# Performance work log

Hardware: AMD Instinct MI355X
Metric: run time of the kernel (lower is better)

The kernel has to match this reference:

```python
import jax, jax.numpy as jnp
import numpy as np

S = 64.0
M = 0.5
EPS = 1e-07
NORM_EPS = 1e-12  # matches torch F.normalize default eps
B, D, C = 512, 512, 64000


def _l2_normalize(a, axis=-1):
    n = jnp.sqrt(jnp.sum(a * a, axis=axis, keepdims=True))
    return a / jnp.maximum(n, NORM_EPS)


def setup_inputs() -> dict:
    key = jax.random.key(0)
    kx, ky, kw = jax.random.split(key, 3)
    x = jax.random.normal(kx, (B, D), dtype=jnp.float32)
    y = jax.random.randint(ky, (B,), 0, C, dtype=jnp.int64)
    # kaiming_uniform-ish init: bound = sqrt(6 / fan_in)
    bound = np.sqrt(6.0 / D).astype(np.float32)
    W = jax.random.uniform(kw, (C, D), dtype=jnp.float32, minval=-bound, maxval=bound)
    return {"x": x, "y": y, "W": W}


def reference(x, y, W):
    # cosine similarities: [B, C]
    theta = _l2_normalize(x) @ _l2_normalize(W).T
    # target logit per row
    tgt = jnp.take_along_axis(theta, y[:, None], axis=1)[:, 0]  # [B]
    numerator = S * jnp.cos(jnp.arccos(jnp.clip(tgt, -1.0 + EPS, 1.0 - EPS)) + M)
    # sum of exp(s*theta) over non-target classes (mask out target column)
    is_tgt = jnp.arange(C, dtype=y.dtype)[None, :] == y[:, None]  # [B, C]
    excl_sum = jnp.sum(jnp.where(is_tgt, 0.0, jnp.exp(S * theta)), axis=1)  # [B]
    denominator = jnp.exp(numerator) + excl_sum
    return -jnp.mean(numerator - jnp.log(denominator))
```

## Files before the change

### kernel.cpp

```cpp
#include <hip/hip_runtime.h>


#define B_N 512
#define D_N 512
#define C_N 64000
#define S_SCALE 64.0f
#define MARGIN 0.5f
#define EPS_C 1e-7f
#define NREP 16

typedef unsigned short ushort_t;
typedef __attribute__((ext_vector_type(8))) short short8;
typedef __attribute__((ext_vector_type(4))) float floatx4;
typedef __attribute__((ext_vector_type(4))) float fvec4;

__device__ __forceinline__ ushort_t f2bf(float f) {
    unsigned int u = __float_as_uint(f);
    u += 0x7fffu + ((u >> 16) & 1u);
    return (ushort_t)(u >> 16);
}

__global__ void xprep_kernel(const float* __restrict__ x,
                             ushort_t* __restrict__ xnT,
                             float* __restrict__ rowsumR) {
    int b = blockIdx.x;
    int t = threadIdx.x;
    if (b == 128) {
#pragma unroll
        for (int i = 0; i < NREP * B_N / 256; ++i)
            rowsumR[i * 256 + t] = 0.0f;
        return;
    }
    int row  = b * 4 + (t >> 6);
    int lane = t & 63;
    const float4* p = (const float4*)(x + (size_t)row * D_N);
    float4 v0 = p[lane * 2];
    float4 v1 = p[lane * 2 + 1];
    float ss = v0.x*v0.x + v0.y*v0.y + v0.z*v0.z + v0.w*v0.w
             + v1.x*v1.x + v1.y*v1.y + v1.z*v1.z + v1.w*v1.w;
#pragma unroll
    for (int off = 32; off > 0; off >>= 1) ss += __shfl_xor(ss, off);
    float sc = 1.0f / fmaxf(sqrtf(ss), 1e-12f);
    uint4 o;
    o.x = (unsigned)f2bf(v0.x*sc) | ((unsigned)f2bf(v0.y*sc) << 16);
    o.y = (unsigned)f2bf(v0.z*sc) | ((unsigned)f2bf(v0.w*sc) << 16);
    o.z = (unsigned)f2bf(v1.x*sc) | ((unsigned)f2bf(v1.y*sc) << 16);
    o.w = (unsigned)f2bf(v1.z*sc) | ((unsigned)f2bf(v1.w*sc) << 16);
    *((uint4*)(xnT + ((size_t)(lane << 9) + row) * 8)) = o;
}

__global__ __launch_bounds__(512, 4)
void gemm_fused_kernel(const float* __restrict__ W,
                       const ushort_t* __restrict__ xnT,
                       const int* __restrict__ y,
                       float* __restrict__ rowsumR,
                       float* __restrict__ tgt) {
    __shared__ ushort_t sW[64 * 512];

    int t    = threadIdx.x;
    int lane = t & 63;
    int w    = t >> 6;
    int lq   = lane >> 4;
    int lc   = lane & 15;
    int cn0  = blockIdx.x * 64;

#pragma unroll
    for (int rr = 0; rr < 8; ++rr) {
        int row = w * 8 + rr;
        const fvec4* p = (const fvec4*)(W + (size_t)(cn0 + row) * D_N);
        fvec4 a = __builtin_nontemporal_load(p + lane * 2);
        fvec4 b = __builtin_nontemporal_load(p + lane * 2 + 1);
        float ss = a.x*a.x + a.y*a.y + a.z*a.z + a.w*a.w
                 + b.x*b.x + b.y*b.y + b.z*b.z + b.w*b.w;
#pragma unroll
        for (int off = 32; off > 0; off >>= 1) ss += __shfl_xor(ss, off);
        float sc = 1.0f / fmaxf(sqrtf(ss), 1e-12f);
        uint4 o;
        o.x = (unsigned)f2bf(a.x*sc) | ((unsigned)f2bf(a.y*sc) << 16);
        o.y = (unsigned)f2bf(a.z*sc) | ((unsigned)f2bf(a.w*sc) << 16);
        o.z = (unsigned)f2bf(b.x*sc) | ((unsigned)f2bf(b.y*sc) << 16);
        o.w = (unsigned)f2bf(b.z*sc) | ((unsigned)f2bf(b.w*sc) << 16);
        int kc = lane;
        int rs = row ^ (kc & 7);
        *((uint4*)(sW + kc * 512 + rs * 8)) = o;
    }
    __syncthreads();

    floatx4 acc[4][4];
#pragma unroll
    for (int i = 0; i < 4; i++)
#pragma unroll
        for (int j = 0; j < 4; j++) acc[i][j] = (floatx4){0.f, 0.f, 0.f, 0.f};

    const ushort_t* apT[4];
#pragma unroll
    for (int tm = 0; tm < 4; tm++)
        apT[tm] = xnT + ((size_t)lq * 512 + w * 64 + tm * 16 + lc) * 8;

    short8 af[4];
#pragma unroll
    for (int tm = 0; tm < 4; tm++) af[tm] = *(const short8*)(apT[tm]);

    for (int k = 0; k < 16; ++k) {
        short8 afn[4];
        if (k < 15) {
#pragma unroll
            for (int tm = 0; tm < 4; tm++)
                afn[tm] = *(const short8*)(apT[tm] + (k + 1) * 16384);
        }
        int kc = k * 4 + lq;
        short8 bfr[4];
#pragma unroll
        for (int tn = 0; tn < 4; tn++) {
            int rs = (tn * 16 + lc) ^ (kc & 7);
            bfr[tn] = *(const short8*)(sW + kc * 512 + rs * 8);
        }
#pragma unroll
        for (int tm = 0; tm < 4; tm++)
#pragma unroll
            for (int tn = 0; tn < 4; tn++)
                acc[tm][tn] = __builtin_amdgcn_mfma_f32_16x16x32_bf16(
                    af[tm], bfr[tn], acc[tm][tn], 0, 0, 0);
        if (k < 15) {
#pragma unroll
            for (int tm = 0; tm < 4; tm++) af[tm] = afn[tm];
        }
    }

    __syncthreads();
    float* rowacc = (float*)sW;
#pragma unroll
    for (int tm = 0; tm < 4; tm++) {
#pragma unroll
        for (int r = 0; r < 4; r++) {
            int lrow = w * 64 + tm * 16 + lq * 4 + r;
            int yv   = y[lrow];
            float esum = 0.0f;
#pragma unroll
            for (int tn = 0; tn < 4; tn++) {
                int gcol = cn0 + tn * 16 + lc;
                float theta = acc[tm][tn][r];
                if (gcol == yv) {
                    tgt[lrow] = theta;
                } else {
                    esum += __expf(S_SCALE * theta);
                }
            }
#pragma unroll
            for (int off = 1; off < 16; off <<= 1) esum += __shfl_xor(esum, off);
            if (lc == 0) rowacc[lrow] = esum;
        }
    }
    __syncthreads();
    atomicAdd(&rowsumR[(blockIdx.x & (NREP - 1)) * B_N + t], rowacc[t]);
}

__global__ void finalize_kernel(const float* __restrict__ rowsumR,
                                const float* __restrict__ tgt,
                                float* __restrict__ out) {
    __shared__ float red[256];
    int t = threadIdx.x;
    float s = 0.0f;
    for (int r = t; r < B_N; r += 256) {
        float rs = 0.0f;
#pragma unroll
        for (int i = 0; i < NREP; ++i) rs += rowsumR[i * B_N + r];
        float tv = tgt[r];
        tv = fminf(fmaxf(tv, -1.0f + EPS_C), 1.0f - EPS_C);
        float num = S_SCALE * cosf(acosf(tv) + MARGIN);
        float den = expf(num) + rs;
        s += num - logf(den);
    }
    red[t] = s;
    __syncthreads();
    for (int o = 128; o > 0; o >>= 1) {
        if (t < o) red[t] += red[t + o];
        __syncthreads();
    }
    if (t == 0) out[0] = -red[0] / (float)B_N;
}

extern "C" void kernel_launch(void* const* d_in, const int* in_sizes, int n_in,
                              void* d_out, int out_size, void* d_ws, size_t ws_size,
                              hipStream_t stream) {
    const float* x = (const float*)d_in[0];
    const int*   y = (const int*)d_in[1];
    const float* W = (const float*)d_in[2];
    float* out = (float*)d_out;

    char* ws = (char*)d_ws;
    ushort_t* xnT   = (ushort_t*)ws;
    float* rowsumR  = (float*)(ws + 524288);
    float* tgt      = rowsumR + NREP * B_N;

    xprep_kernel<<<129, 256, 0, stream>>>(x, xnT, rowsumR);
    gemm_fused_kernel<<<C_N / 64, 512, 0, stream>>>(W, xnT, y, rowsumR, tgt);
    finalize_kernel<<<1, 256, 0, stream>>>(rowsumR, tgt, out);
}
```

Before: 221.5 us.

## Process four class tiles per block with double-buffered W prefetch

```diff
diff --git a/kernel.cpp b/kernel.cpp
--- a/kernel.cpp
+++ b/kernel.cpp
@@ -8,6 +8,8 @@
 #define MARGIN 0.5f
 #define EPS_C 1e-7f
 #define NREP 16
+#define TPB 4
+#define GRID_GEMM 250
 
 typedef unsigned short ushort_t;
 typedef __attribute__((ext_vector_type(8))) short short8;
@@ -49,25 +51,36 @@
     *((uint4*)(xnT + ((size_t)(lane << 9) + row) * 8)) = o;
 }
 
-__global__ __launch_bounds__(512, 4)
+__global__ __launch_bounds__(512, 2)
 void gemm_fused_kernel(const float* __restrict__ W,
                        const ushort_t* __restrict__ xnT,
                        const int* __restrict__ y,
                        float* __restrict__ rowsumR,
                        float* __restrict__ tgt) {
-    __shared__ ushort_t sW[64 * 512];
-
-    int t    = threadIdx.x;
-    int lane = t & 63;
-    int w    = t >> 6;
-    int lq   = lane >> 4;
-    int lc   = lane & 15;
-    int cn0  = blockIdx.x * 64;
+    __shared__ ushort_t sW[2][64 * 512];
+
+    int t     = threadIdx.x;
+    int lane  = t & 63;
+    int w     = t >> 6;
+    int lq    = lane >> 4;
+    int lc    = lane & 15;
+    int cbase = blockIdx.x * (TPB * 64);
+
+    const ushort_t* apT[4];
+#pragma unroll
+    for (int tm = 0; tm < 4; tm++)
+        apT[tm] = xnT + ((size_t)lq * 512 + w * 64 + tm * 16 + lc) * 8;
+
+    float esum[4][4];
+#pragma unroll
+    for (int tm = 0; tm < 4; tm++)
+#pragma unroll
+        for (int r = 0; r < 4; r++) esum[tm][r] = 0.0f;
 
 #pragma unroll
     for (int rr = 0; rr < 8; ++rr) {
         int row = w * 8 + rr;
-        const fvec4* p = (const fvec4*)(W + (size_t)(cn0 + row) * D_N);
+        const fvec4* p = (const fvec4*)(W + (size_t)(cbase + row) * D_N);
         fvec4 a = __builtin_nontemporal_load(p + lane * 2);
         fvec4 b = __builtin_nontemporal_load(p + lane * 2 + 1);
         float ss = a.x*a.x + a.y*a.y + a.z*a.z + a.w*a.w
@@ -82,77 +95,126 @@
         o.w = (unsigned)f2bf(b.z*sc) | ((unsigned)f2bf(b.w*sc) << 16);
         int kc = lane;
         int rs = row ^ (kc & 7);
-        *((uint4*)(sW + kc * 512 + rs * 8)) = o;
+        *((uint4*)(&sW[0][kc * 512 + rs * 8])) = o;
     }
     __syncthreads();
 
-    floatx4 acc[4][4];
-#pragma unroll
-    for (int i = 0; i < 4; i++)
-#pragma unroll
-        for (int j = 0; j < 4; j++) acc[i][j] = (floatx4){0.f, 0.f, 0.f, 0.f};
-
-    const ushort_t* apT[4];
-#pragma unroll
-    for (int tm = 0; tm < 4; tm++)
-        apT[tm] = xnT + ((size_t)lq * 512 + w * 64 + tm * 16 + lc) * 8;
-
-    short8 af[4];
-#pragma unroll
-    for (int tm = 0; tm < 4; tm++) af[tm] = *(const short8*)(apT[tm]);
-
-    for (int k = 0; k < 16; ++k) {
-        short8 afn[4];
-        if (k < 15) {
+    int cur = 0;
+    for (int tt = 0; tt < TPB; ++tt) {
+        const int  cn0     = cbase + tt * 64;
+        const bool notlast = (tt < TPB - 1);
+        const ushort_t* sWc = sW[cur];
+        ushort_t*       sWn = sW[cur ^ 1];
+        const int  nb      = cn0 + 64;
+
+        floatx4 acc[4][4];
+#pragma unroll
+        for (int i = 0; i < 4; i++)
+#pragma unroll
+            for (int j = 0; j < 4; j++) acc[i][j] = (floatx4){0.f, 0.f, 0.f, 0.f};
+
+        short8 af[4];
+#pragma unroll
+        for (int tm = 0; tm < 4; tm++) af[tm] = *(const short8*)(apT[tm]);
+
+        fvec4 wA[8], wB[8];
+
+#pragma unroll
+        for (int k = 0; k < 16; ++k) {
+            short8 afn[4];
+            if (k < 15) {
+#pragma unroll
+                for (int tm = 0; tm < 4; tm++)
+                    afn[tm] = *(const short8*)(apT[tm] + (k + 1) * 16384);
+            }
+            if (notlast && (k == 1 || k == 3 || k == 5 || k == 7)) {
+                const int bi = (k - 1) >> 1;
+#pragma unroll
+                for (int rx = 0; rx < 2; ++rx) {
+                    int row = w * 8 + bi * 2 + rx;
+                    const fvec4* p = (const fvec4*)(W + (size_t)(nb + row) * D_N);
+                    wA[bi * 2 + rx] = __builtin_nontemporal_load(p + lane * 2);
+                    wB[bi * 2 + rx] = __builtin_nontemporal_load(p + lane * 2 + 1);
+                }
+            }
+            const int kc = k * 4 + lq;
+            short8 bfr[4];
+#pragma unroll
+            for (int tn = 0; tn < 4; tn++) {
+                int rs = (tn * 16 + lc) ^ (kc & 7);
+                bfr[tn] = *(const short8*)(&sWc[kc * 512 + rs * 8]);
+            }
 #pragma unroll
             for (int tm = 0; tm < 4; tm++)
-                afn[tm] = *(const short8*)(apT[tm] + (k + 1) * 16384);
+#pragma unroll
+                for (int tn = 0; tn < 4; tn++)
+                    acc[tm][tn] = __builtin_amdgcn_mfma_f32_16x16x32_bf16(
+                        af[tm], bfr[tn], acc[tm][tn], 0, 0, 0);
+            if (notlast && (k == 9 || k == 11 || k == 13 || k == 15)) {
+                const int bi = (k - 9) >> 1;
+#pragma unroll
+                for (int rx = 0; rx < 2; ++rx) {
+                    int row = w * 8 + bi * 2 + rx;
+                    fvec4 a = wA[bi * 2 + rx];
+                    fvec4 b = wB[bi * 2 + rx];
+                    float ss = a.x*a.x + a.y*a.y + a.z*a.z + a.w*a.w
+                             + b.x*b.x + b.y*b.y + b.z*b.z + b.w*b.w;
+#pragma unroll
+                    for (int off = 32; off > 0; off >>= 1) ss += __shfl_xor(ss, off);
+                    float sc = 1.0f / fmaxf(sqrtf(ss), 1e-12f);
+                    uint4 o;
+                    o.x = (unsigned)f2bf(a.x*sc) | ((unsigned)f2bf(a.y*sc) << 16);
+                    o.y = (unsigned)f2bf(a.z*sc) | ((unsigned)f2bf(a.w*sc) << 16);
+                    o.z = (unsigned)f2bf(b.x*sc) | ((unsigned)f2bf(b.y*sc) << 16);
+                    o.w = (unsigned)f2bf(b.z*sc) | ((unsigned)f2bf(b.w*sc) << 16);
+                    int kcs = lane;
+                    int rs  = row ^ (kcs & 7);
+                    *((uint4*)(&sWn[kcs * 512 + rs * 8])) = o;
+                }
+            }
+            if (k < 15) {
+#pragma unroll
+                for (int tm = 0; tm < 4; tm++) af[tm] = afn[tm];
+            }
         }
-        int kc = k * 4 + lq;
-        short8 bfr[4];
-#pragma unroll
-        for (int tn = 0; tn < 4; tn++) {
-            int rs = (tn * 16 + lc) ^ (kc & 7);
-            bfr[tn] = *(const short8*)(sW + kc * 512 + rs * 8);
+
+#pragma unroll
+        for (int tm = 0; tm < 4; tm++) {
+#pragma unroll
+            for (int r = 0; r < 4; r++) {
+                int grow = w * 64 + tm * 16 + lq * 4 + r;
+                int yv   = y[grow];
+                float es = 0.0f;
+#pragma unroll
+                for (int tn = 0; tn < 4; tn++) {
+                    int gcol = cn0 + tn * 16 + lc;
+                    float theta = acc[tm][tn][r];
+                    if (gcol == yv) {
+                        tgt[grow] = theta;
+                    } else {
+                        es += __expf(S_SCALE * theta);
+                    }
+                }
+                esum[tm][r] += es;
+            }
         }
-#pragma unroll
-        for (int tm = 0; tm < 4; tm++)
-#pragma unroll
-            for (int tn = 0; tn < 4; tn++)
-                acc[tm][tn] = __builtin_amdgcn_mfma_f32_16x16x32_bf16(
-                    af[tm], bfr[tn], acc[tm][tn], 0, 0, 0);
-        if (k < 15) {
-#pragma unroll
-            for (int tm = 0; tm < 4; tm++) af[tm] = afn[tm];
+        __syncthreads();
+        cur ^= 1;
+    }
+
+#pragma unroll
+    for (int tm = 0; tm < 4; tm++) {
+#pragma unroll
+        for (int r = 0; r < 4; r++) {
+            float e = esum[tm][r];
+#pragma unroll
+            for (int off = 1; off < 16; off <<= 1) e += __shfl_xor(e, off);
+            if (lc == 0) {
+                int grow = w * 64 + tm * 16 + lq * 4 + r;
+                atomicAdd(&rowsumR[(blockIdx.x & (NREP - 1)) * B_N + grow], e);
+            }
         }
     }
-
-    __syncthreads();
-    float* rowacc = (float*)sW;
-#pragma unroll
-    for (int tm = 0; tm < 4; tm++) {
-#pragma unroll
-        for (int r = 0; r < 4; r++) {
-            int lrow = w * 64 + tm * 16 + lq * 4 + r;
-            int yv   = y[lrow];
-            float esum = 0.0f;
-#pragma unroll
-            for (int tn = 0; tn < 4; tn++) {
-                int gcol = cn0 + tn * 16 + lc;
-                float theta = acc[tm][tn][r];
-                if (gcol == yv) {
-                    tgt[lrow] = theta;
-                } else {
-                    esum += __expf(S_SCALE * theta);
-                }
-            }
-#pragma unroll
-            for (int off = 1; off < 16; off <<= 1) esum += __shfl_xor(esum, off);
-            if (lc == 0) rowacc[lrow] = esum;
-        }
-    }
-    __syncthreads();
-    atomicAdd(&rowsumR[(blockIdx.x & (NREP - 1)) * B_N + t], rowacc[t]);
 }
 
 __global__ void finalize_kernel(const float* __restrict__ rowsumR,
@@ -194,6 +256,6 @@
     float* tgt      = rowsumR + NREP * B_N;
 
     xprep_kernel<<<129, 256, 0, stream>>>(x, xnT, rowsumR);
-    gemm_fused_kernel<<<C_N / 64, 512, 0, stream>>>(W, xnT, y, rowsumR, tgt);
+    gemm_fused_kernel<<<GRID_GEMM, 512, 0, stream>>>(W, xnT, y, rowsumR, tgt);
     finalize_kernel<<<1, 256, 0, stream>>>(rowsumR, tgt, out);
 }
```

Result: slower. 396.6 us (+79.1%).

## Shrink GEMM tile to 32 classes per block and defer W normalization

Applied to the files above, without the earlier changes.

```diff
diff --git a/kernel.cpp b/kernel.cpp
--- a/kernel.cpp
+++ b/kernel.cpp
@@ -8,6 +8,8 @@
 #define MARGIN 0.5f
 #define EPS_C 1e-7f
 #define NREP 16
+#define TILE_C 32
+#define GRID_GEMM 2000
 
 typedef unsigned short ushort_t;
 typedef __attribute__((ext_vector_type(8))) short short8;
@@ -49,20 +51,22 @@
     *((uint4*)(xnT + ((size_t)(lane << 9) + row) * 8)) = o;
 }
 
-__global__ __launch_bounds__(512, 4)
+__global__ __launch_bounds__(256, 4)
 void gemm_fused_kernel(const float* __restrict__ W,
                        const ushort_t* __restrict__ xnT,
                        const int* __restrict__ y,
                        float* __restrict__ rowsumR,
                        float* __restrict__ tgt) {
-    __shared__ ushort_t sW[64 * 512];
+    __shared__ ushort_t sW[64 * 256];
+    __shared__ float    norms2[TILE_C];
 
     int t    = threadIdx.x;
     int lane = t & 63;
     int w    = t >> 6;
     int lq   = lane >> 4;
     int lc   = lane & 15;
-    int cn0  = blockIdx.x * 64;
+    int cn0  = blockIdx.x * TILE_C;
+    int rep  = blockIdx.x & (NREP - 1);
 
 #pragma unroll
     for (int rr = 0; rr < 8; ++rr) {
@@ -74,85 +78,82 @@
                  + b.x*b.x + b.y*b.y + b.z*b.z + b.w*b.w;
 #pragma unroll
         for (int off = 32; off > 0; off >>= 1) ss += __shfl_xor(ss, off);
-        float sc = 1.0f / fmaxf(sqrtf(ss), 1e-12f);
         uint4 o;
-        o.x = (unsigned)f2bf(a.x*sc) | ((unsigned)f2bf(a.y*sc) << 16);
-        o.y = (unsigned)f2bf(a.z*sc) | ((unsigned)f2bf(a.w*sc) << 16);
-        o.z = (unsigned)f2bf(b.x*sc) | ((unsigned)f2bf(b.y*sc) << 16);
-        o.w = (unsigned)f2bf(b.z*sc) | ((unsigned)f2bf(b.w*sc) << 16);
-        int kc = lane;
-        int rs = row ^ (kc & 7);
-        *((uint4*)(sW + kc * 512 + rs * 8)) = o;
+        o.x = (unsigned)f2bf(a.x) | ((unsigned)f2bf(a.y) << 16);
+        o.y = (unsigned)f2bf(a.z) | ((unsigned)f2bf(a.w) << 16);
+        o.z = (unsigned)f2bf(b.x) | ((unsigned)f2bf(b.y) << 16);
+        o.w = (unsigned)f2bf(b.z) | ((unsigned)f2bf(b.w) << 16);
+        *((uint4*)(&sW[lane * 256 + (row ^ (lane & 7)) * 8])) = o;
+        if (lane == 0) norms2[row] = ss;
     }
     __syncthreads();
 
-    floatx4 acc[4][4];
-#pragma unroll
-    for (int i = 0; i < 4; i++)
-#pragma unroll
-        for (int j = 0; j < 4; j++) acc[i][j] = (floatx4){0.f, 0.f, 0.f, 0.f};
-
-    const ushort_t* apT[4];
-#pragma unroll
-    for (int tm = 0; tm < 4; tm++)
-        apT[tm] = xnT + ((size_t)lq * 512 + w * 64 + tm * 16 + lc) * 8;
-
-    short8 af[4];
-#pragma unroll
-    for (int tm = 0; tm < 4; tm++) af[tm] = *(const short8*)(apT[tm]);
+    const ushort_t* abase = xnT + ((size_t)lq * 512 + (size_t)w * 128 + lc) * 8;
+
+    floatx4 acc[8][2];
+#pragma unroll
+    for (int i = 0; i < 8; i++)
+#pragma unroll
+        for (int j = 0; j < 2; j++) acc[i][j] = (floatx4){0.f, 0.f, 0.f, 0.f};
+
+    short8 af[8], afn[8];
+#pragma unroll
+    for (int tm = 0; tm < 8; tm++)
+        af[tm] = *(const short8*)(abase + tm * 128);
 
     for (int k = 0; k < 16; ++k) {
-        short8 afn[4];
         if (k < 15) {
 #pragma unroll
-            for (int tm = 0; tm < 4; tm++)
-                afn[tm] = *(const short8*)(apT[tm] + (k + 1) * 16384);
+            for (int tm = 0; tm < 8; tm++)
+                afn[tm] = *(const short8*)(abase + (size_t)(k + 1) * 16384 + tm * 128);
         }
         int kc = k * 4 + lq;
-        short8 bfr[4];
-#pragma unroll
-        for (int tn = 0; tn < 4; tn++) {
+        short8 bfr[2];
+#pragma unroll
+        for (int tn = 0; tn < 2; tn++) {
             int rs = (tn * 16 + lc) ^ (kc & 7);
-            bfr[tn] = *(const short8*)(sW + kc * 512 + rs * 8);
-        }
-#pragma unroll
-        for (int tm = 0; tm < 4; tm++)
-#pragma unroll
-            for (int tn = 0; tn < 4; tn++)
+            bfr[tn] = *(const short8*)(&sW[kc * 256 + rs * 8]);
+        }
+#pragma unroll
+        for (int tm = 0; tm < 8; tm++)
+#pragma unroll
+            for (int tn = 0; tn < 2; tn++)
                 acc[tm][tn] = __builtin_amdgcn_mfma_f32_16x16x32_bf16(
                     af[tm], bfr[tn], acc[tm][tn], 0, 0, 0);
         if (k < 15) {
 #pragma unroll
-            for (int tm = 0; tm < 4; tm++) af[tm] = afn[tm];
-        }
-    }
-
-    __syncthreads();
-    float* rowacc = (float*)sW;
-#pragma unroll
-    for (int tm = 0; tm < 4; tm++) {
+            for (int tm = 0; tm < 8; tm++) af[tm] = afn[tm];
+        }
+    }
+
+    float rn[2];
+#pragma unroll
+    for (int tn = 0; tn < 2; tn++)
+        rn[tn] = 1.0f / fmaxf(sqrtf(norms2[tn * 16 + lc]), 1e-12f);
+
+#pragma unroll
+    for (int tm = 0; tm < 8; tm++) {
 #pragma unroll
         for (int r = 0; r < 4; r++) {
-            int lrow = w * 64 + tm * 16 + lq * 4 + r;
-            int yv   = y[lrow];
-            float esum = 0.0f;
-#pragma unroll
-            for (int tn = 0; tn < 4; tn++) {
+            int grow = w * 128 + tm * 16 + lq * 4 + r;
+            int yv   = y[grow];
+            float es = 0.0f;
+#pragma unroll
+            for (int tn = 0; tn < 2; tn++) {
                 int gcol = cn0 + tn * 16 + lc;
-                float theta = acc[tm][tn][r];
+                float theta = acc[tm][tn][r] * rn[tn];
                 if (gcol == yv) {
-                    tgt[lrow] = theta;
+                    tgt[grow] = theta;
                 } else {
-                    esum += __expf(S_SCALE * theta);
+                    es += __expf(S_SCALE * theta);
                 }
             }
 #pragma unroll
-            for (int off = 1; off < 16; off <<= 1) esum += __shfl_xor(esum, off);
-            if (lc == 0) rowacc[lrow] = esum;
-        }
-    }
-    __syncthreads();
-    atomicAdd(&rowsumR[(blockIdx.x & (NREP - 1)) * B_N + t], rowacc[t]);
+            for (int off = 1; off < 16; off <<= 1) es += __shfl_xor(es, off);
+            if (lc == 0)
+                atomicAdd(&rowsumR[rep * B_N + grow], es);
+        }
+    }
 }
 
 __global__ void finalize_kernel(const float* __restrict__ rowsumR,
@@ -194,6 +195,6 @@
     float* tgt      = rowsumR + NREP * B_N;
 
     xprep_kernel<<<129, 256, 0, stream>>>(x, xnT, rowsumR);
-    gemm_fused_kernel<<<C_N / 64, 512, 0, stream>>>(W, xnT, y, rowsumR, tgt);
+    gemm_fused_kernel<<<GRID_GEMM, 256, 0, stream>>>(W, xnT, y, rowsumR, tgt);
     finalize_kernel<<<1, 256, 0, stream>>>(rowsumR, tgt, out);
 }
```

After: 263.9 us. +19.2%, slower.

## Use persistent warp-specialized GEMM blocks with double-buffered W tiles

Applied to the files above, without the earlier changes.

```diff
diff --git a/kernel.cpp b/kernel.cpp
--- a/kernel.cpp
+++ b/kernel.cpp
@@ -8,6 +8,10 @@
 #define MARGIN 0.5f
 #define EPS_C 1e-7f
 #define NREP 16
+#define TPB 4
+#define GRID_GEMM 250
+#define NCONS 8
+#define NTHREADS 640
 
 typedef unsigned short ushort_t;
 typedef __attribute__((ext_vector_type(8))) short short8;
@@ -49,110 +53,160 @@
     *((uint4*)(xnT + ((size_t)(lane << 9) + row) * 8)) = o;
 }
 
-__global__ __launch_bounds__(512, 4)
+__global__ __launch_bounds__(NTHREADS, 2)
 void gemm_fused_kernel(const float* __restrict__ W,
                        const ushort_t* __restrict__ xnT,
                        const int* __restrict__ y,
                        float* __restrict__ rowsumR,
                        float* __restrict__ tgt) {
-    __shared__ ushort_t sW[64 * 512];
-
-    int t    = threadIdx.x;
-    int lane = t & 63;
-    int w    = t >> 6;
-    int lq   = lane >> 4;
-    int lc   = lane & 15;
-    int cn0  = blockIdx.x * 64;
-
-#pragma unroll
-    for (int rr = 0; rr < 8; ++rr) {
-        int row = w * 8 + rr;
-        const fvec4* p = (const fvec4*)(W + (size_t)(cn0 + row) * D_N);
-        fvec4 a = __builtin_nontemporal_load(p + lane * 2);
-        fvec4 b = __builtin_nontemporal_load(p + lane * 2 + 1);
-        float ss = a.x*a.x + a.y*a.y + a.z*a.z + a.w*a.w
-                 + b.x*b.x + b.y*b.y + b.z*b.z + b.w*b.w;
-#pragma unroll
-        for (int off = 32; off > 0; off >>= 1) ss += __shfl_xor(ss, off);
-        float sc = 1.0f / fmaxf(sqrtf(ss), 1e-12f);
-        uint4 o;
-        o.x = (unsigned)f2bf(a.x*sc) | ((unsigned)f2bf(a.y*sc) << 16);
-        o.y = (unsigned)f2bf(a.z*sc) | ((unsigned)f2bf(a.w*sc) << 16);
-        o.z = (unsigned)f2bf(b.x*sc) | ((unsigned)f2bf(b.y*sc) << 16);
-        o.w = (unsigned)f2bf(b.z*sc) | ((unsigned)f2bf(b.w*sc) << 16);
-        int kc = lane;
-        int rs = row ^ (kc & 7);
-        *((uint4*)(sW + kc * 512 + rs * 8)) = o;
+    __shared__ ushort_t sW[2][64 * 512];
+    __shared__ float    norms2[2][64];
+
+    const int t    = threadIdx.x;
+    const int lane = t & 63;
+    const int w    = t >> 6;
+    const int lq   = lane >> 4;
+    const int lc   = lane & 15;
+    const int cbase = blockIdx.x * (TPB * 64);
+    const int rep   = blockIdx.x & (NREP - 1);
+
+    if (w < NCONS) {
+#pragma unroll 4
+        for (int rr = 0; rr < 8; ++rr) {
+            int row = w * 8 + rr;
+            const fvec4* p = (const fvec4*)(W + (size_t)(cbase + row) * D_N);
+            fvec4 a = __builtin_nontemporal_load(p + lane * 2);
+            fvec4 b = __builtin_nontemporal_load(p + lane * 2 + 1);
+            float ss = a.x*a.x + a.y*a.y + a.z*a.z + a.w*a.w
+                     + b.x*b.x + b.y*b.y + b.z*b.z + b.w*b.w;
+#pragma unroll
+            for (int off = 32; off > 0; off >>= 1) ss += __shfl_xor(ss, off);
+            uint4 o;
+            o.x = (unsigned)f2bf(a.x) | ((unsigned)f2bf(a.y) << 16);
+            o.y = (unsigned)f2bf(a.z) | ((unsigned)f2bf(a.w) << 16);
+            o.z = (unsigned)f2bf(b.x) | ((unsigned)f2bf(b.y) << 16);
+            o.w = (unsigned)f2bf(b.z) | ((unsigned)f2bf(b.w) << 16);
+            *((uint4*)(&sW[0][lane * 512 + (row ^ (lane & 7)) * 8])) = o;
+            if (lane == 0) norms2[0][row] = ss;
+        }
     }
     __syncthreads();
 
-    floatx4 acc[4][4];
-#pragma unroll
-    for (int i = 0; i < 4; i++)
-#pragma unroll
-        for (int j = 0; j < 4; j++) acc[i][j] = (floatx4){0.f, 0.f, 0.f, 0.f};
-
-    const ushort_t* apT[4];
-#pragma unroll
-    for (int tm = 0; tm < 4; tm++)
-        apT[tm] = xnT + ((size_t)lq * 512 + w * 64 + tm * 16 + lc) * 8;
-
-    short8 af[4];
-#pragma unroll
-    for (int tm = 0; tm < 4; tm++) af[tm] = *(const short8*)(apT[tm]);
-
-    for (int k = 0; k < 16; ++k) {
-        short8 afn[4];
-        if (k < 15) {
+    int cur = 0;
+#pragma unroll 1
+    for (int tt = 0; tt < TPB; ++tt) {
+        const int cn0 = cbase + tt * 64;
+        const ushort_t* sWc = &sW[cur][0];
+        const float*    n2c = &norms2[cur][0];
+
+        if (w < NCONS) {
+            const ushort_t* apT[4];
 #pragma unroll
             for (int tm = 0; tm < 4; tm++)
-                afn[tm] = *(const short8*)(apT[tm] + (k + 1) * 16384);
+                apT[tm] = xnT + ((size_t)lq * 512 + w * 64 + tm * 16 + lc) * 8;
+
+            floatx4 acc[4][4];
+#pragma unroll
+            for (int i = 0; i < 4; i++)
+#pragma unroll
+                for (int j = 0; j < 4; j++)
+                    acc[i][j] = (floatx4){0.f, 0.f, 0.f, 0.f};
+
+            short8 af[4], afn[4];
+#pragma unroll
+            for (int tm = 0; tm < 4; tm++) af[tm] = *(const short8*)(apT[tm]);
+
+            for (int k = 0; k < 16; ++k) {
+                if (k < 15) {
+#pragma unroll
+                    for (int tm = 0; tm < 4; tm++)
+                        afn[tm] = *(const short8*)(apT[tm] + (k + 1) * 16384);
+                }
+                int kc = k * 4 + lq;
+                short8 bfr[4];
+#pragma unroll
+                for (int tn = 0; tn < 4; tn++) {
+                    int rs = (tn * 16 + lc) ^ (kc & 7);
+                    bfr[tn] = *(const short8*)(&sWc[kc * 512 + rs * 8]);
+                }
+#pragma unroll
+                for (int tm = 0; tm < 4; tm++)
+#pragma unroll
+                    for (int tn = 0; tn < 4; tn++)
+                        acc[tm][tn] = __builtin_amdgcn_mfma_f32_16x16x32_bf16(
+                            af[tm], bfr[tn], acc[tm][tn], 0, 0, 0);
+                if (k < 15) {
+#pragma unroll
+                    for (int tm = 0; tm < 4; tm++) af[tm] = afn[tm];
+                }
+            }
+
+            float rn[4];
+#pragma unroll
+            for (int tn = 0; tn < 4; tn++)
+                rn[tn] = 1.0f / fmaxf(sqrtf(n2c[tn * 16 + lc]), 1e-12f);
+#pragma unroll
+            for (int tm = 0; tm < 4; tm++) {
+#pragma unroll
+                for (int r = 0; r < 4; r++) {
+                    int grow = w * 64 + tm * 16 + lq * 4 + r;
+                    int yv   = y[grow];
+                    float es = 0.0f;
+#pragma unroll
+                    for (int tn = 0; tn < 4; tn++) {
+                        int gcol = cn0 + tn * 16 + lc;
+                        float theta = acc[tm][tn][r] * rn[tn];
+                        if (gcol == yv) {
+                            tgt[grow] = theta;
+                        } else {
+                            es += __expf(S_SCALE * theta);
+                        }
+                    }
+#pragma unroll
+                    for (int off = 1; off < 16; off <<= 1)
+                        es += __shfl_xor(es, off);
+                    if (lc == 0)
+                        atomicAdd(&rowsumR[rep * B_N + grow], es);
+                }
+            }
+        } else if (tt < TPB - 1) {
+            ushort_t* sWn = &sW[cur ^ 1][0];
+            float*    n2n = &norms2[cur ^ 1][0];
+            const int nb  = cn0 + 64;
+            const int r0  = (w - NCONS) * 32;
+#pragma unroll 1
+            for (int rb = 0; rb < 32; rb += 8) {
+                fvec4 av[8], bv[8];
+#pragma unroll
+                for (int j = 0; j < 8; ++j) {
+                    const fvec4* p =
+                        (const fvec4*)(W + (size_t)(nb + r0 + rb + j) * D_N);
+                    av[j] = __builtin_nontemporal_load(p + lane * 2);
+                    bv[j] = __builtin_nontemporal_load(p + lane * 2 + 1);
+                }
+#pragma unroll
+                for (int j = 0; j < 8; ++j) {
+                    int row = r0 + rb + j;
+                    fvec4 a = av[j];
+                    fvec4 b = bv[j];
+                    float ss = a.x*a.x + a.y*a.y + a.z*a.z + a.w*a.w
+                             + b.x*b.x + b.y*b.y + b.z*b.z + b.w*b.w;
+#pragma unroll
+                    for (int off = 32; off > 0; off >>= 1)
+                        ss += __shfl_xor(ss, off);
+                    uint4 o;
+                    o.x = (unsigned)f2bf(a.x) | ((unsigned)f2bf(a.y) << 16);
+                    o.y = (unsigned)f2bf(a.z) | ((unsigned)f2bf(a.w) << 16);
+                    o.z = (unsigned)f2bf(b.x) | ((unsigned)f2bf(b.y) << 16);
+                    o.w = (unsigned)f2bf(b.z) | ((unsigned)f2bf(b.w) << 16);
+                    *((uint4*)(&sWn[lane * 512 + (row ^ (lane & 7)) * 8])) = o;
+                    if (lane == 0) n2n[row] = ss;
+                }
+            }
         }
-        int kc = k * 4 + lq;
-        short8 bfr[4];
-#pragma unroll
-        for (int tn = 0; tn < 4; tn++) {
-            int rs = (tn * 16 + lc) ^ (kc & 7);
-            bfr[tn] = *(const short8*)(sW + kc * 512 + rs * 8);
-        }
-#pragma unroll
-        for (int tm = 0; tm < 4; tm++)
-#pragma unroll
-            for (int tn = 0; tn < 4; tn++)
-                acc[tm][tn] = __builtin_amdgcn_mfma_f32_16x16x32_bf16(
-                    af[tm], bfr[tn], acc[tm][tn], 0, 0, 0);
-        if (k < 15) {
-#pragma unroll
-            for (int tm = 0; tm < 4; tm++) af[tm] = afn[tm];
-        }
-    }
-
-    __syncthreads();
-    float* rowacc = (float*)sW;
-#pragma unroll
-    for (int tm = 0; tm < 4; tm++) {
-#pragma unroll
-        for (int r = 0; r < 4; r++) {
-            int lrow = w * 64 + tm * 16 + lq * 4 + r;
-            int yv   = y[lrow];
-            float esum = 0.0f;
-#pragma unroll
-            for (int tn = 0; tn < 4; tn++) {
-                int gcol = cn0 + tn * 16 + lc;
-                float theta = acc[tm][tn][r];
-                if (gcol == yv) {
-                    tgt[lrow] = theta;
-                } else {
-                    esum += __expf(S_SCALE * theta);
-                }
-            }
-#pragma unroll
-            for (int off = 1; off < 16; off <<= 1) esum += __shfl_xor(esum, off);
-            if (lc == 0) rowacc[lrow] = esum;
-        }
-    }
-    __syncthreads();
-    atomicAdd(&rowsumR[(blockIdx.x & (NREP - 1)) * B_N + t], rowacc[t]);
+        __syncthreads();
+        cur ^= 1;
+    }
 }
 
 __global__ void finalize_kernel(const float* __restrict__ rowsumR,
@@ -194,6 +248,6 @@
     float* tgt      = rowsumR + NREP * B_N;
 
     xprep_kernel<<<129, 256, 0, stream>>>(x, xnT, rowsumR);
-    gemm_fused_kernel<<<C_N / 64, 512, 0, stream>>>(W, xnT, y, rowsumR, tgt);
+    gemm_fused_kernel<<<GRID_GEMM, NTHREADS, 0, stream>>>(W, xnT, y, rowsumR, tgt);
     finalize_kernel<<<1, 256, 0, stream>>>(rowsumR, tgt, out);
 }
```

After: 327.1 us. 1.48x slower.
